# Kernel optimization log

Measured on AMD Instinct MI355X. Metric: run time of the kernel, lower is better.

Reference implementation:

```python
import jax, jax.numpy as jnp
import numpy as np

EPSILON = 0.0

def setup_inputs() -> dict:
    key = jax.random.key(0)
    k1, k2, k3, k4, k5 = jax.random.split(key, 5)
    N, MAX_NB, D_IN, D_OUT, N_BONDS = 50000, 16, 256, 256, 400000
    x = jax.random.normal(k1, (N, D_IN), dtype=jnp.float32)
    W = jax.random.normal(k2, (D_OUT, D_IN), dtype=jnp.float32) * (1.0 / np.sqrt(D_IN))
    b = jax.random.normal(k3, (D_OUT,), dtype=jnp.float32) * 0.01
    b_from_a = jax.random.randint(k4, (N_BONDS,), 0, N, dtype=jnp.int32)
    a_from_b = jax.random.randint(k5, (N, MAX_NB), 0, N_BONDS, dtype=jnp.int32)
    return {"x": x, "W": W, "b": b, "b_from_a": b_from_a, "a_from_b": a_from_b}

def reference(x, W, b, b_from_a, a_from_b):
    # a2a[i, k] = source atom of the k-th neighbor bond of atom i
    a2a = b_from_a[a_from_b]                      # [N, max_nb]
    h = x @ W.T + b                               # [N, d_out]
    h = h.at[0].set(0.0)                          # row 0 is padding
    message = h[a2a]                              # [N, max_nb, d_out] gather
    out = (1.0 + EPSILON) * h + jnp.sum(message, axis=1)
    return jax.nn.relu(out)
```

## Files before the change

kernel.cpp:

```cpp
#include <hip/hip_runtime.h>

typedef short bf16x4 __attribute__((ext_vector_type(4)));
typedef short bf16x8 __attribute__((ext_vector_type(8)));
typedef float f32x4  __attribute__((ext_vector_type(4)));

__device__ __forceinline__ unsigned short f32_to_bf16(float f) {
  union { float f; unsigned int u; } v; v.f = f;
  unsigned int u = v.u;
  u += 0x7fffu + ((u >> 16) & 1u);
  return (unsigned short)(u >> 16);
}
__device__ __forceinline__ float bf16lo_to_f32(unsigned int u) {
  union { unsigned int u; float f; } v; v.u = u << 16; return v.f;
}
__device__ __forceinline__ float bf16hi_to_f32(unsigned int u) {
  union { unsigned int u; float f; } v; v.u = u & 0xffff0000u; return v.f;
}

#define LDP 40
__global__ __launch_bounds__(512, 4) void gin_gemm(
    const float* __restrict__ x, const float* __restrict__ W,
    const float* __restrict__ bias, unsigned short* __restrict__ h, int M) {
  __shared__ __align__(16) unsigned short As[64 * LDP];
  __shared__ __align__(16) unsigned short Bs[256 * LDP];

  const int tid  = threadIdx.x;
  const int wid  = tid >> 6;
  const int lane = tid & 63;
  const int row0 = blockIdx.x * 64;

  f32x4 acc[4][2] = {};

  const int srowA = tid >> 3;
  const int skA   = (tid & 7) << 2;
  int agrow = row0 + srowA;
  if (agrow >= M) agrow = M - 1;
  const float* aRow = x + (size_t)agrow * 256 + skA;
  const int srowB = tid >> 2;
  const int skB   = (tid & 3) << 3;
  const float* bRow = W + (size_t)srowB * 256 + skB;

  for (int kt = 0; kt < 8; ++kt) {
    const int kb = kt * 32;
    {
      float4 v = *(const float4*)(aRow + kb);
      bf16x4 u;
      u[0] = (short)f32_to_bf16(v.x); u[1] = (short)f32_to_bf16(v.y);
      u[2] = (short)f32_to_bf16(v.z); u[3] = (short)f32_to_bf16(v.w);
      *(bf16x4*)(&As[srowA * LDP + skA]) = u;
    }
#pragma unroll
    for (int j = 0; j < 2; ++j) {
      const float* p = bRow + (size_t)(j * 128) * 256 + kb;
      float4 v0 = *(const float4*)p;
      float4 v1 = *(const float4*)(p + 4);
      bf16x8 u;
      u[0] = (short)f32_to_bf16(v0.x); u[1] = (short)f32_to_bf16(v0.y);
      u[2] = (short)f32_to_bf16(v0.z); u[3] = (short)f32_to_bf16(v0.w);
      u[4] = (short)f32_to_bf16(v1.x); u[5] = (short)f32_to_bf16(v1.y);
      u[6] = (short)f32_to_bf16(v1.z); u[7] = (short)f32_to_bf16(v1.w);
      *(bf16x8*)(&Bs[(j * 128 + srowB) * LDP + skB]) = u;
    }
    __syncthreads();

    const int r16 = lane & 15;
    const int qk  = (lane >> 4) << 3;
    bf16x8 af[4], bfr[2];
#pragma unroll
    for (int g = 0; g < 4; ++g)
      af[g] = *(const bf16x8*)(&As[(g * 16 + r16) * LDP + qk]);
#pragma unroll
    for (int g = 0; g < 2; ++g)
      bfr[g] = *(const bf16x8*)(&Bs[(wid * 32 + g * 16 + r16) * LDP + qk]);
#pragma unroll
    for (int rg = 0; rg < 4; ++rg)
#pragma unroll
      for (int cg = 0; cg < 2; ++cg)
        acc[rg][cg] = __builtin_amdgcn_mfma_f32_16x16x32_bf16(
            af[rg], bfr[cg], acc[rg][cg], 0, 0, 0);
    __syncthreads();
  }

  const int quad = lane >> 4;
  const int c16  = lane & 15;
#pragma unroll
  for (int rg = 0; rg < 4; ++rg) {
#pragma unroll
    for (int r = 0; r < 4; ++r) {
      int grow = row0 + rg * 16 + quad * 4 + r;
      if (grow >= M) continue;
#pragma unroll
      for (int cg = 0; cg < 2; ++cg) {
        int col = wid * 32 + cg * 16 + c16;
        float v = acc[rg][cg][r] + bias[col];
        if (grow == 0) v = 0.0f;
        h[(size_t)grow * 256 + col] = f32_to_bf16(v);
      }
    }
  }
}

__global__ __launch_bounds__(256, 4) void gin_gather(
    const unsigned short* __restrict__ h, const int* __restrict__ b_from_a,
    const int* __restrict__ a_from_b, float* __restrict__ out, int N) {
  const int tid  = threadIdx.x;
  const int wid  = tid >> 6;
  const int lane = tid & 63;
  const int half = lane >> 5;
  const int l32  = lane & 31;
  const int i0   = blockIdx.x * 8 + wid * 2;
  if (i0 >= N) return;
  const int row  = i0 + half;
  const int rowc = (row < N) ? row : (N - 1);

  int src = 0;
  if (lane < 32) {
    int idx = i0 * 16 + lane;
    int lim = N * 16 - 1;
    if (idx > lim) idx = lim;
    src = b_from_a[a_from_b[idx]];
  }

  const int c0 = l32 * 8;
  uint4 u = *(const uint4*)(h + (size_t)rowc * 256 + c0);
  float a0 = bf16lo_to_f32(u.x), a1 = bf16hi_to_f32(u.x);
  float a2 = bf16lo_to_f32(u.y), a3 = bf16hi_to_f32(u.y);
  float a4 = bf16lo_to_f32(u.z), a5 = bf16hi_to_f32(u.z);
  float a6 = bf16lo_to_f32(u.w), a7 = bf16hi_to_f32(u.w);

#pragma unroll
  for (int k = 0; k < 16; ++k) {
    int s = __shfl(src, half * 16 + k, 64);
    uint4 v = *(const uint4*)(h + (size_t)s * 256 + c0);
    a0 += bf16lo_to_f32(v.x); a1 += bf16hi_to_f32(v.x);
    a2 += bf16lo_to_f32(v.y); a3 += bf16hi_to_f32(v.y);
    a4 += bf16lo_to_f32(v.z); a5 += bf16hi_to_f32(v.z);
    a6 += bf16lo_to_f32(v.w); a7 += bf16hi_to_f32(v.w);
  }

  if (row < N) {
    f32x4 r0, r1;
    r0[0] = fmaxf(a0, 0.0f); r0[1] = fmaxf(a1, 0.0f);
    r0[2] = fmaxf(a2, 0.0f); r0[3] = fmaxf(a3, 0.0f);
    r1[0] = fmaxf(a4, 0.0f); r1[1] = fmaxf(a5, 0.0f);
    r1[2] = fmaxf(a6, 0.0f); r1[3] = fmaxf(a7, 0.0f);
    float* op = out + (size_t)row * 256 + c0;
    __builtin_nontemporal_store(r0, (f32x4*)op);
    __builtin_nontemporal_store(r1, (f32x4*)(op + 4));
  }
}

extern "C" void kernel_launch(void* const* d_in, const int* in_sizes, int n_in,
                              void* d_out, int out_size, void* d_ws, size_t ws_size,
                              hipStream_t stream) {
  const float* x        = (const float*)d_in[0];
  const float* W        = (const float*)d_in[1];
  const float* b        = (const float*)d_in[2];
  const int*   b_from_a = (const int*)d_in[3];
  const int*   a_from_b = (const int*)d_in[4];
  float*       out      = (float*)d_out;
  const int M = in_sizes[0] / 256;

  unsigned short* h = (unsigned short*)d_ws;

  gin_gemm<<<(M + 63) / 64, 512, 0, stream>>>(x, W, b, h, M);
  gin_gather<<<(M + 7) / 8, 256, 0, stream>>>(h, b_from_a, a_from_b, out, M);
}
```

Measured before the change: 194.0 us.

## Double-buffer LDS tiles in GEMM with register prefetch of next K-slice

The GEMM kernel now keeps two LDS buffers for A and B. While the MFMAs run on the current K-slice, it loads the next slice's fp32 data from global memory into registers, then converts it to bf16 and stores it into the other buffer. This hides global load latency behind compute and cuts the number of barriers per iteration from two to one. In exchange it doubles LDS usage and raises register pressure, which could lower occupancy under the 512x4 launch bound. The gather kernel, likely the dominant cost, is unchanged.

```diff
diff --git a/kernel.cpp b/kernel.cpp
--- a/kernel.cpp
+++ b/kernel.cpp
@@ -16,18 +16,34 @@
 __device__ __forceinline__ float bf16hi_to_f32(unsigned int u) {
   union { unsigned int u; float f; } v; v.u = u & 0xffff0000u; return v.f;
 }
+__device__ __forceinline__ bf16x4 cvt4(float4 v) {
+  bf16x4 u;
+  u[0] = (short)f32_to_bf16(v.x); u[1] = (short)f32_to_bf16(v.y);
+  u[2] = (short)f32_to_bf16(v.z); u[3] = (short)f32_to_bf16(v.w);
+  return u;
+}
+__device__ __forceinline__ bf16x8 cvt8(float4 v0, float4 v1) {
+  bf16x8 u;
+  u[0] = (short)f32_to_bf16(v0.x); u[1] = (short)f32_to_bf16(v0.y);
+  u[2] = (short)f32_to_bf16(v0.z); u[3] = (short)f32_to_bf16(v0.w);
+  u[4] = (short)f32_to_bf16(v1.x); u[5] = (short)f32_to_bf16(v1.y);
+  u[6] = (short)f32_to_bf16(v1.z); u[7] = (short)f32_to_bf16(v1.w);
+  return u;
+}
 
 #define LDP 40
 __global__ __launch_bounds__(512, 4) void gin_gemm(
     const float* __restrict__ x, const float* __restrict__ W,
     const float* __restrict__ bias, unsigned short* __restrict__ h, int M) {
-  __shared__ __align__(16) unsigned short As[64 * LDP];
-  __shared__ __align__(16) unsigned short Bs[256 * LDP];
+  __shared__ __align__(16) unsigned short As[2][64 * LDP];
+  __shared__ __align__(16) unsigned short Bs[2][256 * LDP];
 
   const int tid  = threadIdx.x;
   const int wid  = tid >> 6;
   const int lane = tid & 63;
   const int row0 = blockIdx.x * 64;
+  const int r16  = lane & 15;
+  const int qk   = (lane >> 4) << 3;
 
   f32x4 acc[4][2] = {};
 
@@ -40,45 +56,49 @@
   const int skB   = (tid & 3) << 3;
   const float* bRow = W + (size_t)srowB * 256 + skB;
 
+  {
+    float4 av  = *(const float4*)(aRow);
+    float4 b00 = *(const float4*)(bRow);
+    float4 b01 = *(const float4*)(bRow + 4);
+    float4 b10 = *(const float4*)(bRow + (size_t)128 * 256);
+    float4 b11 = *(const float4*)(bRow + (size_t)128 * 256 + 4);
+    *(bf16x4*)(&As[0][srowA * LDP + skA]) = cvt4(av);
+    *(bf16x8*)(&Bs[0][srowB * LDP + skB]) = cvt8(b00, b01);
+    *(bf16x8*)(&Bs[0][(128 + srowB) * LDP + skB]) = cvt8(b10, b11);
+  }
+  __syncthreads();
+
+#pragma unroll
   for (int kt = 0; kt < 8; ++kt) {
-    const int kb = kt * 32;
-    {
-      float4 v = *(const float4*)(aRow + kb);
-      bf16x4 u;
-      u[0] = (short)f32_to_bf16(v.x); u[1] = (short)f32_to_bf16(v.y);
-      u[2] = (short)f32_to_bf16(v.z); u[3] = (short)f32_to_bf16(v.w);
-      *(bf16x4*)(&As[srowA * LDP + skA]) = u;
+    const int cur = kt & 1;
+    float4 nav, nb00, nb01, nb10, nb11;
+    if (kt < 7) {
+      const int kb = (kt + 1) * 32;
+      nav  = *(const float4*)(aRow + kb);
+      nb00 = *(const float4*)(bRow + kb);
+      nb01 = *(const float4*)(bRow + kb + 4);
+      nb10 = *(const float4*)(bRow + (size_t)128 * 256 + kb);
+      nb11 = *(const float4*)(bRow + (size_t)128 * 256 + kb + 4);
     }
-#pragma unroll
-    for (int j = 0; j < 2; ++j) {
-      const float* p = bRow + (size_t)(j * 128) * 256 + kb;
-      float4 v0 = *(const float4*)p;
-      float4 v1 = *(const float4*)(p + 4);
-      bf16x8 u;
-      u[0] = (short)f32_to_bf16(v0.x); u[1] = (short)f32_to_bf16(v0.y);
-      u[2] = (short)f32_to_bf16(v0.z); u[3] = (short)f32_to_bf16(v0.w);
-      u[4] = (short)f32_to_bf16(v1.x); u[5] = (short)f32_to_bf16(v1.y);
-      u[6] = (short)f32_to_bf16(v1.z); u[7] = (short)f32_to_bf16(v1.w);
-      *(bf16x8*)(&Bs[(j * 128 + srowB) * LDP + skB]) = u;
-    }
-    __syncthreads();
-
-    const int r16 = lane & 15;
-    const int qk  = (lane >> 4) << 3;
     bf16x8 af[4], bfr[2];
 #pragma unroll
     for (int g = 0; g < 4; ++g)
-      af[g] = *(const bf16x8*)(&As[(g * 16 + r16) * LDP + qk]);
+      af[g] = *(const bf16x8*)(&As[cur][(g * 16 + r16) * LDP + qk]);
 #pragma unroll
     for (int g = 0; g < 2; ++g)
-      bfr[g] = *(const bf16x8*)(&Bs[(wid * 32 + g * 16 + r16) * LDP + qk]);
+      bfr[g] = *(const bf16x8*)(&Bs[cur][(wid * 32 + g * 16 + r16) * LDP + qk]);
 #pragma unroll
     for (int rg = 0; rg < 4; ++rg)
 #pragma unroll
       for (int cg = 0; cg < 2; ++cg)
         acc[rg][cg] = __builtin_amdgcn_mfma_f32_16x16x32_bf16(
             af[rg], bfr[cg], acc[rg][cg], 0, 0, 0);
-    __syncthreads();
+    if (kt < 7) {
+      *(bf16x4*)(&As[cur ^ 1][srowA * LDP + skA]) = cvt4(nav);
+      *(bf16x8*)(&Bs[cur ^ 1][srowB * LDP + skB]) = cvt8(nb00, nb01);
+      *(bf16x8*)(&Bs[cur ^ 1][(128 + srowB) * LDP + skB]) = cvt8(nb10, nb11);
+      __syncthreads();
+    }
   }
 
   const int quad = lane >> 4;
```

Measured after the change: 194.0 us. No clear change (-0.0%).
